# Performance work log

Measured on AMD Instinct MI355X. Metric: run time of the kernel, lower is better.

The kernel has to match this reference:

```python
import jax, jax.numpy as jnp
import numpy as np

N, E, G = 100000, 600000, 4096   # nodes, edges, graphs
D, L = 128, 3                    # emb_dim, num_layer
AV, BV = 100, 8                  # atom / bond categorical vocab sizes
BN_EPS = 1e-5


def _batchnorm(h, g, b):
    # training-mode BatchNorm1d over the node/row axis
    m = h.mean(axis=0)
    v = h.var(axis=0)
    return g * (h - m) / jnp.sqrt(v + BN_EPS) + b


def _reg_mask(mask, seg, size):
    key_num = jax.ops.segment_sum(mask, seg, num_segments=size) + 1e-8
    env_num = jax.ops.segment_sum(1.0 - mask, seg, num_segments=size) + 1e-8
    return key_num, env_num


def setup_inputs() -> dict:
    key = jax.random.key(0)
    ks = jax.random.split(key, 16)
    s = 0.02
    inp = {
        "x": jax.random.randint(ks[0], (N, 9), 0, AV),
        "edge_index": jax.random.randint(ks[1], (2, E), 0, N),
        "edge_attr": jax.random.randint(ks[2], (E, 3), 0, BV),
        "batch": jnp.sort(jax.random.randint(ks[3], (N,), 0, G)),
        # AtomEncoder: 9 embedding tables summed
        "atom_tables": jax.random.normal(ks[4], (9, AV, D), jnp.float32) * s,
        # per-layer BondEncoder: 3 tables each
        "bond_tables": jax.random.normal(ks[5], (L, 3, BV, D), jnp.float32) * s,
        "eps": jnp.zeros((L,), jnp.float32),
        "W1": jax.random.normal(ks[6], (L, D, 2 * D), jnp.float32) * s,
        "b1": jnp.zeros((L, 2 * D), jnp.float32),
        "bn1_g": jnp.ones((L, 2 * D), jnp.float32),
        "bn1_b": jnp.zeros((L, 2 * D), jnp.float32),
        "W2": jax.random.normal(ks[7], (L, 2 * D, D), jnp.float32) * s,
        "b2": jnp.zeros((L, D), jnp.float32),
        "obn_g": jnp.ones((L, D), jnp.float32),
        "obn_b": jnp.zeros((L, D), jnp.float32),
        "node_att_W": jax.random.normal(ks[8], (D, 1), jnp.float32) * s,
        "node_att_b": jnp.zeros((1,), jnp.float32),
        "edge_att_W": jax.random.normal(ks[9], (2 * D, 1), jnp.float32) * s,
        "edge_att_b": jnp.zeros((1,), jnp.float32),
    }
    return inp


def reference(x, edge_index, edge_attr, batch, atom_tables, bond_tables, eps,
              W1, b1, bn1_g, bn1_b, W2, b2, obn_g, obn_b,
              node_att_W, node_att_b, edge_att_W, edge_att_b):
    row, col = edge_index[0], edge_index[1]
    # AtomEncoder: sum of 9 per-feature embeddings -> [N, D]
    h = atom_tables[jnp.arange(9)[None, :], x].sum(axis=1)

    for l in range(L):
        # BondEncoder for this layer -> [E, D]
        e_emb = bond_tables[l][jnp.arange(3)[None, :], edge_attr].sum(axis=1)
        # message: relu(x_j + edge_emb), aggregate (add) at target nodes
        msg = jax.nn.relu(h[row] + e_emb)
        agg = jax.ops.segment_sum(msg, col, num_segments=N)
        z = (1.0 + eps[l]) * h + agg
        # GIN MLP: Linear -> BN -> ReLU -> Linear
        z = jax.nn.relu(_batchnorm(z @ W1[l] + b1[l], bn1_g[l], bn1_b[l]))
        z = z @ W2[l] + b2[l]
        # outer BatchNorm; inter-layer activation; residual (dropout is no-op in eval)
        z = _batchnorm(z, obn_g[l], obn_b[l])
        if l < L - 1:
            z = jax.nn.relu(z)
        h = z + h

    node_rep = h
    edge_rep = jnp.concatenate([node_rep[row], node_rep[col]], axis=-1)  # [E, 2D]
    node_key = jax.nn.sigmoid(node_rep @ node_att_W + node_att_b)        # [N, 1]
    edge_key = jax.nn.sigmoid(edge_rep @ edge_att_W + edge_att_b)        # [E, 1]

    node_key_num, node_env_num = _reg_mask(node_key, batch, G)
    edge_key_num, edge_env_num = _reg_mask(edge_key, batch[row], G)
    return (node_key, edge_key, node_key_num, node_env_num, edge_key_num, edge_env_num)
```

## Files before the change

### kernel.cpp

```cpp
#include <hip/hip_runtime.h>
#include <math.h>

#define N_NODES 100000
#define N_EDGES 600000
#define N_GRAPHS 4096
#define SCAN_CHUNK 512
#define SCAN_NBLK 196
#define EOUT_BLK 512

typedef __attribute__((ext_vector_type(8))) short short8v;
typedef __attribute__((ext_vector_type(4))) float f32x4;

__device__ __forceinline__ unsigned int pack2(float a, float b) {
    unsigned int r;
    asm("v_cvt_pk_bf16_f32 %0, %1, %2" : "=v"(r) : "v"(a), "v"(b));
    return r;
}
__device__ __forceinline__ unsigned short bf16_rne(float f) {
    unsigned int r;
    asm("v_cvt_pk_bf16_f32 %0, %1, %2" : "=v"(r) : "v"(f), "v"(f));
    return (unsigned short)r;
}
__device__ __forceinline__ float bf2f(unsigned short u) {
    return __uint_as_float(((unsigned int)u) << 16);
}

__global__ void k_atom_encode(const int* __restrict__ x, const float* __restrict__ at,
                              unsigned short* __restrict__ hb) {
    int n = blockIdx.x * 2 + (threadIdx.x >> 7);
    int d = threadIdx.x & 127;
    if (n >= N_NODES) return;
    const int* xr = x + n * 9;
    float s = 0.f;
#pragma unroll
    for (int f = 0; f < 9; ++f) {
        int v = xr[f];
        s += at[(f * 100 + v) * 128 + d];
    }
    hb[(size_t)n * 128 + d] = bf16_rne(s);
}

__global__ void k_bondc(const float* __restrict__ bt, unsigned short* __restrict__ ct) {
    int idx = blockIdx.x * 256 + threadIdx.x;
    if (idx >= 3 * 512 * 128) return;
    int d = idx & 127;
    int c = (idx >> 7) & 511;
    int l = idx >> 16;
    const float* base = bt + (size_t)l * 3072;
    float v = base[(c >> 6) * 128 + d] + base[1024 + ((c >> 3) & 7) * 128 + d] +
              base[2048 + (c & 7) * 128 + d];
    ct[idx] = bf16_rne(v);
}

__global__ void k_hist(const int* __restrict__ ei, int* __restrict__ cnt) {
    int e = blockIdx.x * 256 + threadIdx.x;
    if (e < N_EDGES) atomicAdd(&cnt[ei[N_EDGES + e]], 1);
}

__global__ void k_scan_partial(const int* __restrict__ cnt, int* __restrict__ bsum) {
    __shared__ int ls[256];
    int base = blockIdx.x * SCAN_CHUNK;
    int t = threadIdx.x;
    int s = 0;
    for (int i = base + t; i < base + SCAN_CHUNK && i < N_NODES; i += 256) s += cnt[i];
    ls[t] = s;
    __syncthreads();
    for (int off = 128; off; off >>= 1) {
        if (t < off) ls[t] += ls[t + off];
        __syncthreads();
    }
    if (t == 0) bsum[blockIdx.x] = ls[0];
}

__global__ void k_scan_bsum(int* __restrict__ bsum, int* __restrict__ rowptr) {
    __shared__ int ls[256];
    int t = threadIdx.x;
    int v = (t < SCAN_NBLK) ? bsum[t] : 0;
    ls[t] = v;
    __syncthreads();
    for (int off = 1; off < 256; off <<= 1) {
        int x = (t >= off) ? ls[t - off] : 0;
        __syncthreads();
        ls[t] += x;
        __syncthreads();
    }
    if (t < SCAN_NBLK) bsum[t] = ls[t] - v;
    if (t == 255) rowptr[N_NODES] = ls[255];
}

__global__ __launch_bounds__(512) void k_scan_final(const int* __restrict__ bsum,
                                                    int* __restrict__ cnt_cursor,
                                                    int* __restrict__ rowptr) {
    __shared__ int ls[512];
    int base = blockIdx.x * SCAN_CHUNK;
    int t = threadIdx.x;
    int i = base + t;
    int v = (i < N_NODES) ? cnt_cursor[i] : 0;
    ls[t] = v;
    __syncthreads();
    for (int off = 1; off < 512; off <<= 1) {
        int x = (t >= off) ? ls[t - off] : 0;
        __syncthreads();
        ls[t] += x;
        __syncthreads();
    }
    if (i < N_NODES) {
        int excl = bsum[blockIdx.x] + ls[t] - v;
        rowptr[i] = excl;
        cnt_cursor[i] = excl;
    }
}

__global__ void k_fill(const int* __restrict__ ei, const int* __restrict__ ea,
                       int* __restrict__ cursor,
                       int* __restrict__ csr_row, int* __restrict__ csr_attr) {
    int e = blockIdx.x * 256 + threadIdx.x;
    if (e < N_EDGES) {
        int c = ei[N_EDGES + e];
        int pos = atomicAdd(&cursor[c], 1);
        csr_row[pos] = ei[e];
        csr_attr[pos] = ea[e * 3] * 64 + ea[e * 3 + 1] * 8 + ea[e * 3 + 2];
    }
}

__global__ void k_convw(const float* __restrict__ W1, const float* __restrict__ W2,
                        unsigned short* __restrict__ Bp1, unsigned short* __restrict__ Bp2) {
    int idx = blockIdx.x * 256 + threadIdx.x;
    if (idx < 3 * 128 * 256) {
        int l = idx >> 15, r = idx & 32767;
        int k = r >> 8, j = r & 255;
        float v = W1[(size_t)l * 32768 + k * 256 + j];
        Bp1[(size_t)l * 32768 + (((k >> 5) * 4 + ((k >> 3) & 3)) * 256 + j) * 8 + (k & 7)] =
            bf16_rne(v);
    } else if (idx < 6 * 128 * 256) {
        int t = idx - 98304;
        int l = t >> 15, r = t & 32767;
        int k = r >> 7, j = r & 127;
        float v = W2[(size_t)l * 32768 + k * 128 + j];
        Bp2[(size_t)l * 32768 + (((k >> 5) * 4 + ((k >> 3) & 3)) * 128 + j) * 8 + (k & 7)] =
            bf16_rne(v);
    }
}

__global__ void k_gather(const unsigned short* __restrict__ hb,
                         const int* __restrict__ csr_row, const int* __restrict__ csr_attr,
                         const int* __restrict__ rowptr, const unsigned short* __restrict__ ct,
                         const float* __restrict__ eps, int l,
                         unsigned short* __restrict__ zb) {
    int lane = threadIdx.x & 63;
    int n = blockIdx.x * 4 + (threadIdx.x >> 6);
    if (n >= N_NODES) return;
    int i0 = rowptr[n], i1 = rowptr[n + 1];
    float ax = 0.f, ay = 0.f;
    for (int base = i0; base < i1; base += 8) {
        int rr[8], qq[8];
#pragma unroll
        for (int k = 0; k < 8; ++k) {
            int idx = min(base + k, i1 - 1);
            rr[k] = csr_row[idx];
            qq[k] = csr_attr[idx];
        }
        unsigned int u[8], c[8];
#pragma unroll
        for (int k = 0; k < 8; ++k) {
            u[k] = ((const unsigned int*)(hb + (size_t)rr[k] * 128))[lane];
            c[k] = ((const unsigned int*)(ct + qq[k] * 128))[lane];
        }
#pragma unroll
        for (int k = 0; k < 8; ++k) {
            float mk = (base + k < i1) ? 1.f : 0.f;
            float vx = fmaxf(bf2f((unsigned short)(u[k] & 0xffffu)) +
                             bf2f((unsigned short)(c[k] & 0xffffu)), 0.f);
            float vy = fmaxf(bf2f((unsigned short)(u[k] >> 16)) +
                             bf2f((unsigned short)(c[k] >> 16)), 0.f);
            ax = fmaf(mk, vx, ax);
            ay = fmaf(mk, vy, ay);
        }
    }
    float el = 1.0f + eps[l];
    unsigned int un = ((const unsigned int*)(hb + (size_t)n * 128))[lane];
    float zx = fmaf(el, bf2f((unsigned short)(un & 0xffffu)), ax);
    float zy = fmaf(el, bf2f((unsigned short)(un >> 16)), ay);
    ((unsigned int*)(zb + (size_t)n * 128))[lane] = pack2(zx, zy);
}

__global__ __launch_bounds__(256) void k_gemm1(
    const unsigned short* __restrict__ zb, const unsigned short* __restrict__ Bp,
    const float* __restrict__ bias, unsigned short* __restrict__ tb,
    float* __restrict__ sl) {
    __shared__ unsigned short As[8192] __attribute__((aligned(16)));
    int n0 = blockIdx.x * 64;
#pragma unroll
    for (int s = 0; s < 4; ++s) {
        int i = threadIdx.x + s * 256;
        int r = i >> 4, k8 = i & 15;
        short8v v = (short8v)(short)0;
        if (n0 + r < N_NODES) v = ((const short8v*)(zb + (size_t)(n0 + r) * 128))[k8];
        int frag = (r >> 4) * 16 + k8;
        int off = (frag * 128 + (r & 15) * 8) ^ ((k8 & 7) << 3);
        *(short8v*)(&As[off]) = v;
    }
    __syncthreads();
    int lane = threadIdx.x & 63;
    int wid = threadIdx.x >> 6;
    int l15 = lane & 15, kg = lane >> 4;
    int colbase = wid * 64;
    f32x4 acc[4][4];
#pragma unroll
    for (int a = 0; a < 4; ++a)
#pragma unroll
        for (int b = 0; b < 4; ++b) acc[a][b] = (f32x4)(0.f);
#pragma unroll
    for (int k4 = 0; k4 < 4; ++k4) {
        short8v af[4], bf[4];
#pragma unroll
        for (int rb = 0; rb < 4; ++rb)
            af[rb] = *(const short8v*)(&As[((rb * 16 + k4 * 4 + kg) * 128 + l15 * 8) ^
                                           (((k4 * 4 + kg) & 7) << 3)]);
#pragma unroll
        for (int cf = 0; cf < 4; ++cf)
            bf[cf] = *(const short8v*)(Bp + ((k4 * 4 + kg) * 256 + colbase + cf * 16 + l15) * 8);
#pragma unroll
        for (int rb = 0; rb < 4; ++rb)
#pragma unroll
            for (int cf = 0; cf < 4; ++cf)
                acc[rb][cf] = __builtin_amdgcn_mfma_f32_16x16x32_bf16(bf[cf], af[rb],
                                                                      acc[rb][cf], 0, 0, 0);
    }
    float s4[4][4], q4[4][4];
#pragma unroll
    for (int cf = 0; cf < 4; ++cf)
#pragma unroll
        for (int r = 0; r < 4; ++r) { s4[cf][r] = 0.f; q4[cf][r] = 0.f; }
#pragma unroll
    for (int cf = 0; cf < 4; ++cf) {
        int j0 = colbase + cf * 16 + kg * 4;
        float4 b4 = *(const float4*)(bias + j0);
#pragma unroll
        for (int rb = 0; rb < 4; ++rb) {
            int gr = n0 + rb * 16 + l15;
            if (gr < N_NODES) {
                float v0 = acc[rb][cf][0] + b4.x;
                float v1 = acc[rb][cf][1] + b4.y;
                float v2 = acc[rb][cf][2] + b4.z;
                float v3 = acc[rb][cf][3] + b4.w;
                uint2 st;
                st.x = pack2(v0, v1);
                st.y = pack2(v2, v3);
                *(uint2*)(tb + (size_t)gr * 256 + j0) = st;
                s4[cf][0] += v0; q4[cf][0] += v0 * v0;
                s4[cf][1] += v1; q4[cf][1] += v1 * v1;
                s4[cf][2] += v2; q4[cf][2] += v2 * v2;
                s4[cf][3] += v3; q4[cf][3] += v3 * v3;
            }
        }
    }
    float* stats = sl + (size_t)(blockIdx.x & 15) * 768;
    float* part = (float*)As;
    __syncthreads();
#pragma unroll
    for (int cf = 0; cf < 4; ++cf)
#pragma unroll
        for (int r = 0; r < 4; ++r)
            part[(colbase + cf * 16 + kg * 4 + r) * 16 + l15] = s4[cf][r];
    __syncthreads();
    {
        int j = threadIdx.x;
        const float4* pr = (const float4*)(part + j * 16);
        float4 a0 = pr[0], a1 = pr[1], a2 = pr[2], a3 = pr[3];
        float s = a0.x + a0.y + a0.z + a0.w + a1.x + a1.y + a1.z + a1.w +
                  a2.x + a2.y + a2.z + a2.w + a3.x + a3.y + a3.z + a3.w;
        atomicAdd(&stats[j], s);
    }
    __syncthreads();
#pragma unroll
    for (int cf = 0; cf < 4; ++cf)
#pragma unroll
        for (int r = 0; r < 4; ++r)
            part[(colbase + cf * 16 + kg * 4 + r) * 16 + l15] = q4[cf][r];
    __syncthreads();
    {
        int j = threadIdx.x;
        const float4* pr = (const float4*)(part + j * 16);
        float4 a0 = pr[0], a1 = pr[1], a2 = pr[2], a3 = pr[3];
        float s = a0.x + a0.y + a0.z + a0.w + a1.x + a1.y + a1.z + a1.w +
                  a2.x + a2.y + a2.z + a2.w + a3.x + a3.y + a3.z + a3.w;
        atomicAdd(&stats[256 + j], s);
    }
}

__global__ __launch_bounds__(256) void k_gemm2(
    const unsigned short* __restrict__ tb, const unsigned short* __restrict__ Bp,
    const float* __restrict__ sl, const float* __restrict__ g1,
    const float* __restrict__ b1g,
    const float* __restrict__ bias, unsigned short* __restrict__ ub,
    float* __restrict__ slw) {
    __shared__ unsigned short As[16384] __attribute__((aligned(16)));
    int n0 = blockIdx.x * 64;
    int tid = threadIdx.x;
    {
        float* sfin = (float*)As;
        float s = 0.f, q = 0.f;
#pragma unroll
        for (int cc = 0; cc < 16; ++cc) {
            s += sl[cc * 768 + tid];
            q += sl[cc * 768 + 256 + tid];
        }
        float m = s * (1.0f / N_NODES);
        float var = q * (1.0f / N_NODES) - m * m;
        float sc = g1[tid] / sqrtf(var + 1e-5f);
        sfin[tid] = sc;
        sfin[256 + tid] = b1g[tid] - m * sc;
    }
    __syncthreads();
    int kb = (tid & 31) * 8;
    float scr[8], shr[8];
    {
        const float* sfin = (const float*)As;
#pragma unroll
        for (int j = 0; j < 8; ++j) {
            scr[j] = sfin[kb + j];
            shr[j] = sfin[256 + kb + j];
        }
    }
    __syncthreads();
#pragma unroll
    for (int s = 0; s < 8; ++s) {
        int i = tid + s * 256;
        int r = i >> 5, k8 = i & 31;
        short8v v = (short8v)(short)0;
        if (n0 + r < N_NODES) v = ((const short8v*)(tb + (size_t)(n0 + r) * 256))[k8];
        float f0 = fmaxf(fmaf(scr[0], bf2f((unsigned short)v[0]), shr[0]), 0.f);
        float f1 = fmaxf(fmaf(scr[1], bf2f((unsigned short)v[1]), shr[1]), 0.f);
        float f2 = fmaxf(fmaf(scr[2], bf2f((unsigned short)v[2]), shr[2]), 0.f);
        float f3 = fmaxf(fmaf(scr[3], bf2f((unsigned short)v[3]), shr[3]), 0.f);
        float f4 = fmaxf(fmaf(scr[4], bf2f((unsigned short)v[4]), shr[4]), 0.f);
        float f5 = fmaxf(fmaf(scr[5], bf2f((unsigned short)v[5]), shr[5]), 0.f);
        float f6 = fmaxf(fmaf(scr[6], bf2f((unsigned short)v[6]), shr[6]), 0.f);
        float f7 = fmaxf(fmaf(scr[7], bf2f((unsigned short)v[7]), shr[7]), 0.f);
        uint4 ov;
        ov.x = pack2(f0, f1); ov.y = pack2(f2, f3);
        ov.z = pack2(f4, f5); ov.w = pack2(f6, f7);
        int frag = (r >> 4) * 32 + k8;
        int off = (frag * 128 + (r & 15) * 8) ^ ((k8 & 7) << 3);
        *(uint4*)(&As[off]) = ov;
    }
    __syncthreads();
    int lane = threadIdx.x & 63;
    int wid = threadIdx.x >> 6;
    int l15 = lane & 15, kg = lane >> 4;
    int colbase = wid * 32;
    f32x4 acc[4][2];
#pragma unroll
    for (int a = 0; a < 4; ++a) {
        acc[a][0] = (f32x4)(0.f);
        acc[a][1] = (f32x4)(0.f);
    }
#pragma unroll
    for (int k4 = 0; k4 < 8; ++k4) {
        short8v af[4], bf[2];
#pragma unroll
        for (int rb = 0; rb < 4; ++rb)
            af[rb] = *(const short8v*)(&As[((rb * 32 + k4 * 4 + kg) * 128 + l15 * 8) ^
                                           (((k4 * 4 + kg) & 7) << 3)]);
#pragma unroll
        for (int cf = 0; cf < 2; ++cf)
            bf[cf] = *(const short8v*)(Bp + ((k4 * 4 + kg) * 128 + colbase + cf * 16 + l15) * 8);
#pragma unroll
        for (int rb = 0; rb < 4; ++rb)
#pragma unroll
            for (int cf = 0; cf < 2; ++cf)
                acc[rb][cf] = __builtin_amdgcn_mfma_f32_16x16x32_bf16(bf[cf], af[rb],
                                                                      acc[rb][cf], 0, 0, 0);
    }
    float s4[2][4], q4[2][4];
#pragma unroll
    for (int cf = 0; cf < 2; ++cf)
#pragma unroll
        for (int r = 0; r < 4; ++r) { s4[cf][r] = 0.f; q4[cf][r] = 0.f; }
#pragma unroll
    for (int cf = 0; cf < 2; ++cf) {
        int j0 = colbase + cf * 16 + kg * 4;
        float4 b4 = *(const float4*)(bias + j0);
#pragma unroll
        for (int rb = 0; rb < 4; ++rb) {
            int gr = n0 + rb * 16 + l15;
            if (gr < N_NODES) {
                float v0 = acc[rb][cf][0] + b4.x;
                float v1 = acc[rb][cf][1] + b4.y;
                float v2 = acc[rb][cf][2] + b4.z;
                float v3 = acc[rb][cf][3] + b4.w;
                uint2 st;
                st.x = pack2(v0, v1);
                st.y = pack2(v2, v3);
                *(uint2*)(ub + (size_t)gr * 128 + j0) = st;
                s4[cf][0] += v0; q4[cf][0] += v0 * v0;
                s4[cf][1] += v1; q4[cf][1] += v1 * v1;
                s4[cf][2] += v2; q4[cf][2] += v2 * v2;
                s4[cf][3] += v3; q4[cf][3] += v3 * v3;
            }
        }
    }
    float* stats = slw + (size_t)(blockIdx.x & 15) * 768;
    float* part = (float*)As;
    __syncthreads();
#pragma unroll
    for (int cf = 0; cf < 2; ++cf)
#pragma unroll
        for (int r = 0; r < 4; ++r)
            part[(colbase + cf * 16 + kg * 4 + r) * 16 + l15] = s4[cf][r];
    __syncthreads();
    if (tid < 128) {
        const float4* pr = (const float4*)(part + tid * 16);
        float4 a0 = pr[0], a1 = pr[1], a2 = pr[2], a3 = pr[3];
        float s = a0.x + a0.y + a0.z + a0.w + a1.x + a1.y + a1.z + a1.w +
                  a2.x + a2.y + a2.z + a2.w + a3.x + a3.y + a3.z + a3.w;
        atomicAdd(&stats[512 + tid], s);
    }
    __syncthreads();
#pragma unroll
    for (int cf = 0; cf < 2; ++cf)
#pragma unroll
        for (int r = 0; r < 4; ++r)
            part[(colbase + cf * 16 + kg * 4 + r) * 16 + l15] = q4[cf][r];
    __syncthreads();
    if (tid < 128) {
        const float4* pr = (const float4*)(part + tid * 16);
        float4 a0 = pr[0], a1 = pr[1], a2 = pr[2], a3 = pr[3];
        float s = a0.x + a0.y + a0.z + a0.w + a1.x + a1.y + a1.z + a1.w +
                  a2.x + a2.y + a2.z + a2.w + a3.x + a3.y + a3.z + a3.w;
        atomicAdd(&stats[640 + tid], s);
    }
}

__global__ void k_update_h(unsigned short* __restrict__ hb,
                           const unsigned short* __restrict__ ub,
                           const float* __restrict__ sl,
                           const float* __restrict__ g2, const float* __restrict__ b2g,
                           int relu, int head,
                           const int* __restrict__ batch, const float* __restrict__ nW,
                           const float* __restrict__ nb, const float* __restrict__ eW,
                           float* __restrict__ out, float* __restrict__ p,
                           float* __restrict__ q, float* __restrict__ nsc) {
    __shared__ float sfin[256];
    if (threadIdx.x < 128) {
        int j = threadIdx.x;
        float s = 0.f, qq = 0.f;
#pragma unroll
        for (int cc = 0; cc < 16; ++cc) {
            s += sl[cc * 768 + 512 + j];
            qq += sl[cc * 768 + 640 + j];
        }
        float m = s * (1.0f / N_NODES);
        float var = qq * (1.0f / N_NODES) - m * m;
        float sc = g2[j] / sqrtf(var + 1e-5f);
        sfin[j] = sc;
        sfin[128 + j] = b2g[j] - m * sc;
    }
    __syncthreads();
    int kb = (threadIdx.x & 15) * 8;
    float scr[8], shr[8];
#pragma unroll
    for (int j = 0; j < 8; ++j) {
        scr[j] = sfin[kb + j];
        shr[j] = sfin[128 + kb + j];
    }
    int i = blockIdx.x * 256 + threadIdx.x;
    uint4 uv = ((const uint4*)ub)[i];
    uint4 hv = ((const uint4*)hb)[i];
    float v0 = fmaf(scr[0], bf2f((unsigned short)(uv.x & 0xffffu)), shr[0]);
    float v1 = fmaf(scr[1], bf2f((unsigned short)(uv.x >> 16)), shr[1]);
    float v2 = fmaf(scr[2], bf2f((unsigned short)(uv.y & 0xffffu)), shr[2]);
    float v3 = fmaf(scr[3], bf2f((unsigned short)(uv.y >> 16)), shr[3]);
    float v4 = fmaf(scr[4], bf2f((unsigned short)(uv.z & 0xffffu)), shr[4]);
    float v5 = fmaf(scr[5], bf2f((unsigned short)(uv.z >> 16)), shr[5]);
    float v6 = fmaf(scr[6], bf2f((unsigned short)(uv.w & 0xffffu)), shr[6]);
    float v7 = fmaf(scr[7], bf2f((unsigned short)(uv.w >> 16)), shr[7]);
    if (relu) {
        v0 = fmaxf(v0, 0.f); v1 = fmaxf(v1, 0.f); v2 = fmaxf(v2, 0.f); v3 = fmaxf(v3, 0.f);
        v4 = fmaxf(v4, 0.f); v5 = fmaxf(v5, 0.f); v6 = fmaxf(v6, 0.f); v7 = fmaxf(v7, 0.f);
    }
    float h0 = bf2f((unsigned short)(hv.x & 0xffffu)) + v0;
    float h1 = bf2f((unsigned short)(hv.x >> 16)) + v1;
    float h2 = bf2f((unsigned short)(hv.y & 0xffffu)) + v2;
    float h3 = bf2f((unsigned short)(hv.y >> 16)) + v3;
    float h4 = bf2f((unsigned short)(hv.z & 0xffffu)) + v4;
    float h5 = bf2f((unsigned short)(hv.z >> 16)) + v5;
    float h6 = bf2f((unsigned short)(hv.w & 0xffffu)) + v6;
    float h7 = bf2f((unsigned short)(hv.w >> 16)) + v7;
    uint4 hp;
    hp.x = pack2(h0, h1); hp.y = pack2(h2, h3);
    hp.z = pack2(h4, h5); hp.w = pack2(h6, h7);
    ((uint4*)hb)[i] = hp;
    if (head) {
        float4 wn0 = *(const float4*)(nW + kb);
        float4 wn1 = *(const float4*)(nW + kb + 4);
        float4 wa0 = *(const float4*)(eW + kb);
        float4 wa1 = *(const float4*)(eW + kb + 4);
        float4 wb0 = *(const float4*)(eW + 128 + kb);
        float4 wb1 = *(const float4*)(eW + 128 + kb + 4);
        float pn = h0 * wn0.x + h1 * wn0.y + h2 * wn0.z + h3 * wn0.w +
                   h4 * wn1.x + h5 * wn1.y + h6 * wn1.z + h7 * wn1.w;
        float pa = h0 * wa0.x + h1 * wa0.y + h2 * wa0.z + h3 * wa0.w +
                   h4 * wa1.x + h5 * wa1.y + h6 * wa1.z + h7 * wa1.w;
        float pb = h0 * wb0.x + h1 * wb0.y + h2 * wb0.z + h3 * wb0.w +
                   h4 * wb1.x + h5 * wb1.y + h6 * wb1.z + h7 * wb1.w;
#pragma unroll
        for (int off = 1; off < 16; off <<= 1) {
            pn += __shfl_xor(pn, off);
            pa += __shfl_xor(pa, off);
            pb += __shfl_xor(pb, off);
        }
        if ((threadIdx.x & 15) == 0) {
            int gr = i >> 4;
            float nk = 1.f / (1.f + expf(-(pn + nb[0])));
            out[gr] = nk;
            int g = batch[gr];
            float* base = nsc + (size_t)(blockIdx.x & 7) * 8192;
            atomicAdd(&base[g], nk);
            atomicAdd(&base[4096 + g], 1.0f - nk);
            p[gr] = pa;
            q[gr] = pb;
        }
    }
}

__global__ __launch_bounds__(256) void k_edge_out(
    const int* __restrict__ ei, const int* __restrict__ batch,
    const float* __restrict__ p, const float* __restrict__ q,
    const float* __restrict__ eb, float* __restrict__ out,
    float* __restrict__ esc) {
    __shared__ float bins[8192];
    for (int i = threadIdx.x; i < 8192; i += 256) bins[i] = 0.f;
    __syncthreads();
    float ebv = eb[0];
    for (int e = blockIdx.x * 256 + threadIdx.x; e < N_EDGES; e += EOUT_BLK * 256) {
        int r = ei[e], c = ei[N_EDGES + e];
        float ek = 1.f / (1.f + expf(-(p[r] + q[c] + ebv)));
        out[N_NODES + e] = ek;
        int g = batch[r];
        atomicAdd(&bins[g], ek);
        atomicAdd(&bins[4096 + g], 1.0f - ek);
    }
    __syncthreads();
    float* dst = esc + (size_t)blockIdx.x * 8192;
    for (int i = threadIdx.x; i < 8192; i += 256) dst[i] = bins[i];
}

__global__ void k_seg_reduce(const float* __restrict__ nsc, const float* __restrict__ esc,
                             float* __restrict__ out) {
    int i = blockIdx.x * 256 + threadIdx.x;
    if (i >= 16384) return;
    float s = 1e-8f;
    if (i < 8192) {
#pragma unroll
        for (int c = 0; c < 8; ++c) s += nsc[c * 8192 + i];
    } else {
        int j = i - 8192;
        for (int c = 0; c < EOUT_BLK; ++c) s += esc[(size_t)c * 8192 + j];
    }
    out[N_NODES + N_EDGES + i] = s;
}

extern "C" void kernel_launch(void* const* d_in, const int* in_sizes, int n_in,
                              void* d_out, int out_size, void* d_ws, size_t ws_size,
                              hipStream_t stream) {
    const int*   x     = (const int*)d_in[0];
    const int*   ei    = (const int*)d_in[1];
    const int*   ea    = (const int*)d_in[2];
    const int*   batch = (const int*)d_in[3];
    const float* at    = (const float*)d_in[4];
    const float* bt    = (const float*)d_in[5];
    const float* eps   = (const float*)d_in[6];
    const float* W1    = (const float*)d_in[7];
    const float* b1    = (const float*)d_in[8];
    const float* bn1g  = (const float*)d_in[9];
    const float* bn1b  = (const float*)d_in[10];
    const float* W2    = (const float*)d_in[11];
    const float* b2    = (const float*)d_in[12];
    const float* obng  = (const float*)d_in[13];
    const float* obnb  = (const float*)d_in[14];
    const float* nW    = (const float*)d_in[15];
    const float* nb    = (const float*)d_in[16];
    const float* eW    = (const float*)d_in[17];
    const float* eb    = (const float*)d_in[18];
    float* out = (float*)d_out;

    float* ws    = (float*)d_ws;
    float* stats = ws;
    float* p     = stats + 3 * 16 * 768;
    float* q     = p + N_NODES;
    float* nsc   = q + N_NODES;
    float* esc   = nsc + 8 * 8192;
    unsigned short* hb  = (unsigned short*)(esc + (size_t)EOUT_BLK * 8192);
    unsigned short* zub = hb + 12800000;
    unsigned short* tb  = zub + 12800000;
    unsigned short* Bp1 = tb + 25600000;
    unsigned short* Bp2 = Bp1 + 3 * 32768;
    unsigned short* ct  = Bp2 + 3 * 32768;
    int* rowptr  = (int*)(ct + 3 * 65536);
    int* cursor  = rowptr + N_NODES + 1;
    int* csr_row = cursor + N_NODES;
    int* csr_attr = csr_row + N_EDGES;
    int* bsum    = csr_attr + N_EDGES;

    hipMemsetAsync(stats, 0, 3 * 16 * 768 * sizeof(float), stream);
    hipMemsetAsync(nsc, 0, 8 * 8192 * sizeof(float), stream);
    hipMemsetAsync(cursor, 0, N_NODES * sizeof(int), stream);
    k_atom_encode<<<50000, 256, 0, stream>>>(x, at, hb);
    k_convw<<<768, 256, 0, stream>>>(W1, W2, Bp1, Bp2);
    k_bondc<<<768, 256, 0, stream>>>(bt, ct);

    k_hist<<<2344, 256, 0, stream>>>(ei, cursor);
    k_scan_partial<<<SCAN_NBLK, 256, 0, stream>>>(cursor, bsum);
    k_scan_bsum<<<1, 256, 0, stream>>>(bsum, rowptr);
    k_scan_final<<<SCAN_NBLK, 512, 0, stream>>>(bsum, cursor, rowptr);
    k_fill<<<2344, 256, 0, stream>>>(ei, ea, cursor, csr_row, csr_attr);

    for (int l = 0; l < 3; ++l) {
        float* sl = stats + (size_t)l * 16 * 768;
        k_gather<<<25000, 256, 0, stream>>>(hb, csr_row, csr_attr, rowptr,
                                            ct + (size_t)l * 65536, eps, l, zub);
        k_gemm1<<<1563, 256, 0, stream>>>(zub, Bp1 + (size_t)l * 32768, b1 + l * 256, tb, sl);
        k_gemm2<<<1563, 256, 0, stream>>>(tb, Bp2 + (size_t)l * 32768, sl,
                                          bn1g + l * 256, bn1b + l * 256,
                                          b2 + l * 128, zub, sl);
        k_update_h<<<6250, 256, 0, stream>>>(hb, zub, sl, obng + l * 128, obnb + l * 128,
                                             (l < 2) ? 1 : 0, (l == 2) ? 1 : 0,
                                             batch, nW, nb, eW, out, p, q, nsc);
    }

    k_edge_out<<<EOUT_BLK, 256, 0, stream>>>(ei, batch, p, q, eb, out, esc);
    k_seg_reduce<<<64, 256, 0, stream>>>(nsc, esc, out);
}
```

Baseline: 543.2 us.

## Pack CSR source and bond attr into one int; scalarize gather indices

```diff
diff --git a/kernel.cpp b/kernel.cpp
--- a/kernel.cpp
+++ b/kernel.cpp
@@ -112,14 +112,13 @@
 }
 
 __global__ void k_fill(const int* __restrict__ ei, const int* __restrict__ ea,
-                       int* __restrict__ cursor,
-                       int* __restrict__ csr_row, int* __restrict__ csr_attr) {
+                       int* __restrict__ cursor, int* __restrict__ csr_pack) {
     int e = blockIdx.x * 256 + threadIdx.x;
     if (e < N_EDGES) {
         int c = ei[N_EDGES + e];
         int pos = atomicAdd(&cursor[c], 1);
-        csr_row[pos] = ei[e];
-        csr_attr[pos] = ea[e * 3] * 64 + ea[e * 3 + 1] * 8 + ea[e * 3 + 2];
+        int attr = ea[e * 3] * 64 + ea[e * 3 + 1] * 8 + ea[e * 3 + 2];
+        csr_pack[pos] = (ei[e] << 9) | attr;
     }
 }
 
@@ -142,46 +141,53 @@
     }
 }
 
+#define EDGE2(uu, cc)                                                          \
+    {                                                                          \
+        ax += fmaxf(bf2f((unsigned short)((uu) & 0xffffu)) +                   \
+                    bf2f((unsigned short)((cc) & 0xffffu)), 0.f);              \
+        ay += fmaxf(bf2f((unsigned short)((uu) >> 16)) +                       \
+                    bf2f((unsigned short)((cc) >> 16)), 0.f);                  \
+    }
+
 __global__ void k_gather(const unsigned short* __restrict__ hb,
-                         const int* __restrict__ csr_row, const int* __restrict__ csr_attr,
+                         const int* __restrict__ csr_pack,
                          const int* __restrict__ rowptr, const unsigned short* __restrict__ ct,
                          const float* __restrict__ eps, int l,
                          unsigned short* __restrict__ zb) {
     int lane = threadIdx.x & 63;
     int n = blockIdx.x * 4 + (threadIdx.x >> 6);
     if (n >= N_NODES) return;
-    int i0 = rowptr[n], i1 = rowptr[n + 1];
+    n = __builtin_amdgcn_readfirstlane(n);
+    int i0 = __builtin_amdgcn_readfirstlane(rowptr[n]);
+    int i1 = __builtin_amdgcn_readfirstlane(rowptr[n + 1]);
     float ax = 0.f, ay = 0.f;
-    for (int base = i0; base < i1; base += 8) {
-        int rr[8], qq[8];
-#pragma unroll
-        for (int k = 0; k < 8; ++k) {
-            int idx = min(base + k, i1 - 1);
-            rr[k] = csr_row[idx];
-            qq[k] = csr_attr[idx];
-        }
-        unsigned int u[8], c[8];
-#pragma unroll
-        for (int k = 0; k < 8; ++k) {
-            u[k] = ((const unsigned int*)(hb + (size_t)rr[k] * 128))[lane];
-            c[k] = ((const unsigned int*)(ct + qq[k] * 128))[lane];
-        }
-#pragma unroll
-        for (int k = 0; k < 8; ++k) {
-            float mk = (base + k < i1) ? 1.f : 0.f;
-            float vx = fmaxf(bf2f((unsigned short)(u[k] & 0xffffu)) +
-                             bf2f((unsigned short)(c[k] & 0xffffu)), 0.f);
-            float vy = fmaxf(bf2f((unsigned short)(u[k] >> 16)) +
-                             bf2f((unsigned short)(c[k] >> 16)), 0.f);
-            ax = fmaf(mk, vx, ax);
-            ay = fmaf(mk, vy, ay);
-        }
+    int i = i0;
+    for (; i + 4 <= i1; i += 4) {
+        int rc0 = __builtin_amdgcn_readfirstlane(csr_pack[i]);
+        int rc1 = __builtin_amdgcn_readfirstlane(csr_pack[i + 1]);
+        int rc2 = __builtin_amdgcn_readfirstlane(csr_pack[i + 2]);
+        int rc3 = __builtin_amdgcn_readfirstlane(csr_pack[i + 3]);
+        unsigned int u0 = ((const unsigned int*)(hb + ((size_t)(rc0 >> 9) << 7)))[lane];
+        unsigned int u1 = ((const unsigned int*)(hb + ((size_t)(rc1 >> 9) << 7)))[lane];
+        unsigned int u2 = ((const unsigned int*)(hb + ((size_t)(rc2 >> 9) << 7)))[lane];
+        unsigned int u3 = ((const unsigned int*)(hb + ((size_t)(rc3 >> 9) << 7)))[lane];
+        unsigned int c0 = ((const unsigned int*)(ct + ((rc0 & 511) << 7)))[lane];
+        unsigned int c1 = ((const unsigned int*)(ct + ((rc1 & 511) << 7)))[lane];
+        unsigned int c2 = ((const unsigned int*)(ct + ((rc2 & 511) << 7)))[lane];
+        unsigned int c3 = ((const unsigned int*)(ct + ((rc3 & 511) << 7)))[lane];
+        EDGE2(u0, c0); EDGE2(u1, c1); EDGE2(u2, c2); EDGE2(u3, c3);
+    }
+    for (; i < i1; ++i) {
+        int rc0 = __builtin_amdgcn_readfirstlane(csr_pack[i]);
+        unsigned int u0 = ((const unsigned int*)(hb + ((size_t)(rc0 >> 9) << 7)))[lane];
+        unsigned int c0 = ((const unsigned int*)(ct + ((rc0 & 511) << 7)))[lane];
+        EDGE2(u0, c0);
     }
     float el = 1.0f + eps[l];
-    unsigned int un = ((const unsigned int*)(hb + (size_t)n * 128))[lane];
+    unsigned int un = ((const unsigned int*)(hb + ((size_t)n << 7)))[lane];
     float zx = fmaf(el, bf2f((unsigned short)(un & 0xffffu)), ax);
     float zy = fmaf(el, bf2f((unsigned short)(un >> 16)), ay);
-    ((unsigned int*)(zb + (size_t)n * 128))[lane] = pack2(zx, zy);
+    ((unsigned int*)(zb + ((size_t)n << 7)))[lane] = pack2(zx, zy);
 }
 
 __global__ __launch_bounds__(256) void k_gemm1(
@@ -600,9 +606,8 @@
     unsigned short* ct  = Bp2 + 3 * 32768;
     int* rowptr  = (int*)(ct + 3 * 65536);
     int* cursor  = rowptr + N_NODES + 1;
-    int* csr_row = cursor + N_NODES;
-    int* csr_attr = csr_row + N_EDGES;
-    int* bsum    = csr_attr + N_EDGES;
+    int* csr_pack = cursor + N_NODES;
+    int* bsum    = csr_pack + N_EDGES;
 
     hipMemsetAsync(stats, 0, 3 * 16 * 768 * sizeof(float), stream);
     hipMemsetAsync(nsc, 0, 8 * 8192 * sizeof(float), stream);
@@ -615,11 +620,11 @@
     k_scan_partial<<<SCAN_NBLK, 256, 0, stream>>>(cursor, bsum);
     k_scan_bsum<<<1, 256, 0, stream>>>(bsum, rowptr);
     k_scan_final<<<SCAN_NBLK, 512, 0, stream>>>(bsum, cursor, rowptr);
-    k_fill<<<2344, 256, 0, stream>>>(ei, ea, cursor, csr_row, csr_attr);
+    k_fill<<<2344, 256, 0, stream>>>(ei, ea, cursor, csr_pack);
 
     for (int l = 0; l < 3; ++l) {
         float* sl = stats + (size_t)l * 16 * 768;
-        k_gather<<<25000, 256, 0, stream>>>(hb, csr_row, csr_attr, rowptr,
+        k_gather<<<25000, 256, 0, stream>>>(hb, csr_pack, rowptr,
                                             ct + (size_t)l * 65536, eps, l, zub);
         k_gemm1<<<1563, 256, 0, stream>>>(zub, Bp1 + (size_t)l * 32768, b1 + l * 256, tb, sl);
         k_gemm2<<<1563, 256, 0, stream>>>(tb, Bp2 + (size_t)l * 32768, sl,
```

After: 513.7 us. -5.4%, faster.
